# Kernel optimization log

Hardware: AMD Instinct MI355X
Metric: run time of the kernel (lower is better)

Reference implementation:

```python
import jax, jax.numpy as jnp
import numpy as np

B, NP, NM, C, H = 4, 256, 128, 128, 128
EPS = 1e-5

def layernorm(x, g, b):
    mu = jnp.mean(x, axis=-1, keepdims=True)
    var = jnp.var(x, axis=-1, keepdims=True)
    return (x - mu) * jax.lax.rsqrt(var + EPS) * g + b

def setup_inputs() -> dict:
    key = jax.random.key(0)
    ks = jax.random.split(key, 16)
    s = lambda d: 1.0 / np.sqrt(d)
    return {
        "z": jax.random.normal(ks[0], (B, NP, NM, C), jnp.float32),
        "z_mask": jnp.ones((B, NP, NM), jnp.float32),
        "pocket_pair": jax.random.normal(ks[1], (B, NP, NP, C), jnp.float32),
        "mol_pair": jax.random.normal(ks[2], (B, NM, NM, C), jnp.float32),
        "ln_g": jnp.ones((C,), jnp.float32), "ln_b": jnp.zeros((C,), jnp.float32),
        "lnh_g": jnp.ones((H,), jnp.float32), "lnh_b": jnp.zeros((H,), jnp.float32),
        "gw1": jax.random.uniform(ks[3], (C, H), jnp.float32, -s(C), s(C)),
        "gb1": jnp.zeros((H,), jnp.float32),
        "gw2": jax.random.uniform(ks[4], (C, H), jnp.float32, -s(C), s(C)),
        "gb2": jnp.zeros((H,), jnp.float32),
        "w1": jax.random.uniform(ks[5], (C, H), jnp.float32, -s(C), s(C)),
        "b1": jnp.zeros((H,), jnp.float32),
        "w2": jax.random.uniform(ks[6], (C, H), jnp.float32, -s(C), s(C)),
        "b2": jnp.zeros((H,), jnp.float32),
        "egw": jax.random.uniform(ks[7], (C, C), jnp.float32, -s(C), s(C)),
        "egb": jnp.zeros((C,), jnp.float32),
        "asw": jax.random.uniform(ks[8], (H, C), jnp.float32, -s(H), s(H)),
        "asb": jnp.zeros((C,), jnp.float32),
    }

def reference(z, z_mask, pocket_pair, mol_pair, ln_g, ln_b, lnh_g, lnh_b,
              gw1, gb1, gw2, gb2, w1, b1, w2, b2, egw, egb, asw, asb):
    m = z_mask[..., None]                      # [b,Np,Nm,1]
    zn = layernorm(z, ln_g, ln_b)              # [b,Np,Nm,C]
    pp = layernorm(pocket_pair, ln_g, ln_b)    # [b,Np,Np,C]
    mp = layernorm(mol_pair, ln_g, ln_b)       # [b,Nm,Nm,C]
    gate1 = lambda x: jax.nn.sigmoid(x @ gw1 + gb1) * (x @ w1 + b1)
    gate2 = lambda x: jax.nn.sigmoid(x @ gw2 + gb2) * (x @ w2 + b2)
    ab1 = gate1(zn) * m                        # [b,Np,Nm,H]
    ab2 = gate2(zn) * m                        # [b,Np,Nm,H]
    ppg = gate2(pp)                            # [b,Np,Np,H]
    mpg = gate1(mp)                            # [b,Nm,Nm,H]
    block1 = jnp.einsum('bikc,bkjc->bijc', ppg, ab1)   # [b,Np,Nm,H]
    block2 = jnp.einsum('bikc,bjkc->bijc', ab2, mpg)   # [b,Np,Nm,H]
    h = layernorm(block1 + block2, lnh_g, lnh_b)
    out = jax.nn.sigmoid(zn @ egw + egb) * (h @ asw + asb) * m
    return out
```

## Files before the change

### kernel.cpp

```cpp
#include <hip/hip_runtime.h>
#include <hip/hip_bf16.h>

#define DEVFN __device__ __forceinline__
using bf16 = __hip_bfloat16;
typedef __attribute__((ext_vector_type(8))) short short8;
typedef __attribute__((ext_vector_type(4))) float f32x4;
typedef __attribute__((ext_vector_type(4))) unsigned short us4;

constexpr int BB = 4, NP = 256, NM = 128, CC = 128, HH = 128;
constexpr float EPS = 1e-5f;

#define MFMA16(a,b,c) __builtin_amdgcn_mfma_f32_16x16x32_bf16((a),(b),(c),0,0,0)

DEVFN unsigned short bfbits(float v){ union{ bf16 b; unsigned short s; } u; u.b = __float2bfloat16(v); return u.s; }
DEVFN float bits2f(unsigned short s){ union{ unsigned int i; float f; } u; u.i = ((unsigned)s) << 16; return u.f; }
DEVFN float sigm(float x){ return 1.0f / (1.0f + __expf(-x)); }

__global__ __launch_bounds__(256)
void prep_weights_kernel(const float* __restrict__ gw1, const float* __restrict__ w1,
                         const float* __restrict__ gw2, const float* __restrict__ w2,
                         const float* __restrict__ egw, const float* __restrict__ asw,
                         bf16* __restrict__ wt)
{
  __shared__ float wl[128][129];
  const int bx = blockIdx.x;
  const float* W = (bx==0)?gw1 : (bx==1)?w1 : (bx==2)?gw2 : (bx==3)?w2 : (bx==4)?egw : asw;
  const int t = threadIdx.x;
  for (int i = 0; i < 16; ++i){
    int idx = t + 256*i;
    int k = idx >> 5, n0 = (idx & 31) * 4;
    float4 v = *reinterpret_cast<const float4*>(W + k*128 + n0);
    wl[k][n0] = v.x; wl[k][n0+1] = v.y; wl[k][n0+2] = v.z; wl[k][n0+3] = v.w;
  }
  __syncthreads();
  short* o = reinterpret_cast<short*>(wt) + bx * 16384;
  const int n = t >> 1, kh = t & 1;
  #pragma unroll
  for (int j = 0; j < 8; ++j){
    short8 p;
    #pragma unroll
    for (int u = 0; u < 8; ++u) p[u] = (short)bfbits(wl[kh*64 + j*8 + u][n]);
    *reinterpret_cast<short8*>(o + n*128 + kh*64 + j*8) = p;
  }
}

struct GateSmem {
  short xs[128*128];
  float lgb[2][128];
  float mu[128], rs[128], mk[128];
};

DEVFN void gate_pass(const char* xb, const float* mk, int t, int b, long rowb, long R,
                     const short* wtg, const short* wtl,
                     const float* __restrict__ bgp, const float* __restrict__ blp,
                     bf16* __restrict__ outp)
{
  const int l = t & 63, w = t >> 6, lr = l & 15, lg = l >> 4;
  const int n0 = w * 32;
  short8 bgf[2][4], blf[2][4];
  #pragma unroll
  for (int nt = 0; nt < 2; ++nt)
    #pragma unroll
    for (int ks = 0; ks < 4; ++ks){
      int n = n0 + nt*16 + lr, ko = ks*32 + lg*8;
      bgf[nt][ks] = *reinterpret_cast<const short8*>(wtg + n*128 + ko);
      blf[nt][ks] = *reinterpret_cast<const short8*>(wtl + n*128 + ko);
    }
  float bgv[2] = { bgp[n0 + lr], bgp[n0 + 16 + lr] };
  float blv[2] = { blp[n0 + lr], blp[n0 + 16 + lr] };
  unsigned short* ob = reinterpret_cast<unsigned short*>(outp);

  for (int mt = 0; mt < 8; ++mt){
    f32x4 zv = {0.f,0.f,0.f,0.f};
    f32x4 ag0 = zv, ag1 = zv, al0 = zv, al1 = zv;
    #pragma unroll
    for (int ks = 0; ks < 4; ++ks){
      int m = mt*16 + lr, ko = ks*32 + lg*8;
      short8 a = *reinterpret_cast<const short8*>(xb + ((m*256 + ko*2) ^ ((m & 7) << 4)));
      ag0 = MFMA16(a, bgf[0][ks], ag0);
      ag1 = MFMA16(a, bgf[1][ks], ag1);
      al0 = MFMA16(a, blf[0][ks], al0);
      al1 = MFMA16(a, blf[1][ks], al1);
    }
    #pragma unroll
    for (int nt = 0; nt < 2; ++nt){
      f32x4 ag = nt ? ag1 : ag0, al = nt ? al1 : al0;
      int h = n0 + nt*16 + lr;
      us4 pk;
      #pragma unroll
      for (int rg = 0; rg < 4; ++rg){
        int rowl = mt*16 + lg*4 + rg;
        float val = sigm(ag[rg] + bgv[nt]) * (al[rg] + blv[nt]) * mk[rowl];
        pk[rg] = bfbits(val);
      }
      *reinterpret_cast<us4*>(ob + (long)(b*128 + h)*R + rowb + mt*16 + lg*4) = pk;
    }
  }
}

DEVFN void eg_pass(const char* xb, int t, int b, long rowb, long R,
                   const short* wtg, const float* __restrict__ bgp, bf16* __restrict__ outp)
{
  const int l = t & 63, w = t >> 6, lr = l & 15, lg = l >> 4;
  const int n0 = w * 32;
  short8 bgf[2][4];
  #pragma unroll
  for (int nt = 0; nt < 2; ++nt)
    #pragma unroll
    for (int ks = 0; ks < 4; ++ks){
      int n = n0 + nt*16 + lr, ko = ks*32 + lg*8;
      bgf[nt][ks] = *reinterpret_cast<const short8*>(wtg + n*128 + ko);
    }
  float bgv[2] = { bgp[n0 + lr], bgp[n0 + 16 + lr] };
  unsigned short* ob = reinterpret_cast<unsigned short*>(outp);

  for (int mt = 0; mt < 8; ++mt){
    f32x4 zv = {0.f,0.f,0.f,0.f};
    f32x4 ag0 = zv, ag1 = zv;
    #pragma unroll
    for (int ks = 0; ks < 4; ++ks){
      int m = mt*16 + lr, ko = ks*32 + lg*8;
      short8 a = *reinterpret_cast<const short8*>(xb + ((m*256 + ko*2) ^ ((m & 7) << 4)));
      ag0 = MFMA16(a, bgf[0][ks], ag0);
      ag1 = MFMA16(a, bgf[1][ks], ag1);
    }
    #pragma unroll
    for (int nt = 0; nt < 2; ++nt){
      f32x4 ag = nt ? ag1 : ag0;
      int h = n0 + nt*16 + lr;
      us4 pk;
      #pragma unroll
      for (int rg = 0; rg < 4; ++rg) pk[rg] = bfbits(sigm(ag[rg] + bgv[nt]));
      *reinterpret_cast<us4*>(ob + (long)(b*128 + h)*R + rowb + mt*16 + lg*4) = pk;
    }
  }
}

template<int NPASS>
__global__ __launch_bounds__(256, 3)
void gate_mfma_kernel(const float* __restrict__ x, const float* __restrict__ mask,
                      const float* __restrict__ lng, const float* __restrict__ lnb,
                      const bf16* __restrict__ wt,
                      int m1g, int m1l, const float* __restrict__ bg1p, const float* __restrict__ bl1p, bf16* __restrict__ o1,
                      int m2g, int m2l, const float* __restrict__ bg2p, const float* __restrict__ bl2p, bf16* __restrict__ o2,
                      const float* __restrict__ bgep, bf16* __restrict__ oe,
                      long R)
{
  __shared__ GateSmem sm;
  const int t = threadIdx.x;
  const long row0 = (long)blockIdx.x * 128;
  const int b = (int)(row0 / R);
  const long rowb = row0 - (long)b * R;

  if (t < 128){
    sm.lgb[0][t] = lng[t];
    sm.lgb[1][t] = lnb[t];
    sm.mk[t] = mask ? mask[row0 + t] : 1.0f;
  }
  const int r = t >> 1, hf = t & 1;
  const float4* xrow = reinterpret_cast<const float4*>(x + (row0 + r)*128 + hf*64);
  float4 vb[16];
  float s = 0.f, ss = 0.f;
  #pragma unroll
  for (int i = 0; i < 16; ++i){
    float4 v = xrow[i]; vb[i] = v;
    s  += v.x + v.y + v.z + v.w;
    ss += v.x*v.x + v.y*v.y + v.z*v.z + v.w*v.w;
  }
  s  += __shfl_xor(s, 1);
  ss += __shfl_xor(ss, 1);
  if (!hf){
    float mu = s * (1.f/128.f);
    float var = ss * (1.f/128.f) - mu*mu;
    sm.mu[r] = mu;
    sm.rs[r] = rsqrtf(var + EPS);
  }
  __syncthreads();
  {
    const float mu = sm.mu[r], rg = sm.rs[r];
    char* xb = reinterpret_cast<char*>(sm.xs);
    #pragma unroll
    for (int j = 0; j < 8; ++j){
      float4 a = vb[2*j], c2 = vb[2*j+1];
      float vv[8] = {a.x, a.y, a.z, a.w, c2.x, c2.y, c2.z, c2.w};
      short8 p;
      #pragma unroll
      for (int u = 0; u < 8; ++u){
        int ch = hf*64 + j*8 + u;
        p[u] = (short)bfbits((vv[u] - mu) * rg * sm.lgb[0][ch] + sm.lgb[1][ch]);
      }
      *reinterpret_cast<short8*>(xb + ((r*256 + hf*128 + j*16) ^ ((r & 7) << 4))) = p;
    }
  }
  __syncthreads();

  const char* xb = reinterpret_cast<const char*>(sm.xs);
  const short* wts = reinterpret_cast<const short*>(wt);
  gate_pass(xb, sm.mk, t, b, rowb, R, wts + m1g*16384, wts + m1l*16384, bg1p, bl1p, o1);
  if (NPASS == 3){
    gate_pass(xb, sm.mk, t, b, rowb, R, wts + m2g*16384, wts + m2l*16384, bg2p, bl2p, o2);
    eg_pass(xb, t, b, rowb, R, wts + 4*16384, bgep, oe);
  }
}

__global__ __launch_bounds__(256, 2)
void einsum_mfma_kernel(const bf16* __restrict__ ppg, const bf16* __restrict__ ab1,
                        const bf16* __restrict__ ab2, const bf16* __restrict__ mpg,
                        float* __restrict__ bsum)
{
  __shared__ short b1t[128*256];
  const int t = threadIdx.x, l = t & 63, w = t >> 6, lr = l & 15, lg = l >> 4;
  const int bc = blockIdx.x;
  const short* A1 = reinterpret_cast<const short*>(ppg) + (long)bc * (NP*NP);
  const short* B1 = reinterpret_cast<const short*>(ab1) + (long)bc * (NP*NM);
  const short* A2 = reinterpret_cast<const short*>(ab2) + (long)bc * (NP*NM);
  const short* B2 = reinterpret_cast<const short*>(mpg) + (long)bc * (NM*NM);

  char* lb = reinterpret_cast<char*>(b1t);
  for (int it = 0; it < 16; ++it){
    int idx = t + 256*it;
    int k = idx >> 4, j0 = (idx & 15) * 8;
    short8 v = *reinterpret_cast<const short8*>(B1 + idx*8);
    #pragma unroll
    for (int u = 0; u < 8; ++u){
      int j = j0 + u;
      *reinterpret_cast<short*>(lb + ((j*512 + k*2) ^ ((j & 7) << 4))) = v[u];
    }
  }
  __syncthreads();

  f32x4 zv = {0.f,0.f,0.f,0.f};
  f32x4 acc[4][8];
  #pragma unroll
  for (int i = 0; i < 4; ++i)
    #pragma unroll
    for (int j = 0; j < 8; ++j) acc[i][j] = zv;

  const int m0 = w * 64;
  for (int ks = 0; ks < 8; ++ks){
    int ko = ks*32 + lg*8;
    short8 af[4];
    #pragma unroll
    for (int mt = 0; mt < 4; ++mt)
      af[mt] = *reinterpret_cast<const short8*>(A1 + (m0 + mt*16 + lr)*256 + ko);
    short8 bf[8];
    #pragma unroll
    for (int nt = 0; nt < 8; ++nt){
      int n = nt*16 + lr;
      bf[nt] = *reinterpret_cast<const short8*>(lb + ((n*512 + ko*2) ^ ((n & 7) << 4)));
    }
    #pragma unroll
    for (int mt = 0; mt < 4; ++mt)
      #pragma unroll
      for (int nt = 0; nt < 8; ++nt)
        acc[mt][nt] = MFMA16(af[mt], bf[nt], acc[mt][nt]);
  }
  for (int ks = 0; ks < 4; ++ks){
    int ko = ks*32 + lg*8;
    short8 af[4];
    #pragma unroll
    for (int mt = 0; mt < 4; ++mt)
      af[mt] = *reinterpret_cast<const short8*>(A2 + (m0 + mt*16 + lr)*128 + ko);
    short8 bf[8];
    #pragma unroll
    for (int nt = 0; nt < 8; ++nt)
      bf[nt] = *reinterpret_cast<const short8*>(B2 + (nt*16 + lr)*128 + ko);
    #pragma unroll
    for (int mt = 0; mt < 4; ++mt)
      #pragma unroll
      for (int nt = 0; nt < 8; ++nt)
        acc[mt][nt] = MFMA16(af[mt], bf[nt], acc[mt][nt]);
  }
  float* out = bsum + (long)bc * (NP*NM);
  #pragma unroll
  for (int mt = 0; mt < 4; ++mt)
    #pragma unroll
    for (int nt = 0; nt < 8; ++nt)
      #pragma unroll
      for (int rg = 0; rg < 4; ++rg)
        out[(m0 + mt*16 + lg*4 + rg)*128 + nt*16 + lr] = acc[mt][nt][rg];
}

__global__ __launch_bounds__(256, 2)
void final_mfma_kernel(const float* __restrict__ bsum, const bf16* __restrict__ eg,
                       const float* __restrict__ mask,
                       const float* __restrict__ lnhg, const float* __restrict__ lnhb,
                       const bf16* __restrict__ wt, const float* __restrict__ asb,
                       float* __restrict__ out)
{
  __shared__ struct {
    float xsT[128][68];
    short xs[64*128];
    float lgb[2][128];
    float ps[4][64], pss[4][64];
    float mu[64], rs[64], mk[64];
  } sm;
  const int t = threadIdx.x, l = t & 63, w = t >> 6, lr = l & 15, lg = l >> 4;
  const long row0 = (long)blockIdx.x * 64;
  const int b = (int)(row0 >> 15);
  const long rowb = row0 & 32767;

  if (t < 128){ sm.lgb[0][t] = lnhg[t]; sm.lgb[1][t] = lnhb[t]; }
  if (t < 64) sm.mk[t] = mask[row0 + t];

  for (int i = 0; i < 8; ++i){
    int idx = t + 256*i;
    int c = idx >> 4, j4 = idx & 15;
    float4 v = *reinterpret_cast<const float4*>(bsum + (long)(b*128 + c)*32768 + rowb + j4*4);
    *reinterpret_cast<float4*>(&sm.xsT[c][j4*4]) = v;
  }
  __syncthreads();
  {
    int ij = t & 63, q = t >> 6;
    float s = 0.f, ss = 0.f;
    #pragma unroll
    for (int k = 0; k < 32; ++k){
      float v = sm.xsT[q*32 + k][ij];
      s += v; ss += v*v;
    }
    sm.ps[q][ij] = s; sm.pss[q][ij] = ss;
  }
  __syncthreads();
  if (t < 64){
    float s  = sm.ps[0][t] + sm.ps[1][t] + sm.ps[2][t] + sm.ps[3][t];
    float ss = sm.pss[0][t] + sm.pss[1][t] + sm.pss[2][t] + sm.pss[3][t];
    float mu = s * (1.f/128.f);
    float var = ss * (1.f/128.f) - mu*mu;
    sm.mu[t] = mu; sm.rs[t] = rsqrtf(var + EPS);
  }
  __syncthreads();
  {
    int ij = t & 63, q = t >> 6;
    float mu = sm.mu[ij], rg = sm.rs[ij];
    char* xb = reinterpret_cast<char*>(sm.xs);
    #pragma unroll
    for (int u = 0; u < 4; ++u){
      short8 p;
      #pragma unroll
      for (int e = 0; e < 8; ++e){
        int c = q*32 + u*8 + e;
        p[e] = (short)bfbits((sm.xsT[c][ij] - mu) * rg * sm.lgb[0][c] + sm.lgb[1][c]);
      }
      *reinterpret_cast<short8*>(xb + ((ij*256 + q*64 + u*16) ^ ((ij & 7) << 4))) = p;
    }
  }
  __syncthreads();

  const short* aswt = reinterpret_cast<const short*>(wt) + 5*16384;
  short8 bfr[8][4];
  #pragma unroll
  for (int nt = 0; nt < 8; ++nt)
    #pragma unroll
    for (int ks = 0; ks < 4; ++ks)
      bfr[nt][ks] = *reinterpret_cast<const short8*>(aswt + (nt*16 + lr)*128 + ks*32 + lg*8);

  f32x4 zv = {0.f,0.f,0.f,0.f};
  f32x4 acc[8];
  #pragma unroll
  for (int i = 0; i < 8; ++i) acc[i] = zv;
  const char* xb = reinterpret_cast<const char*>(sm.xs);
  #pragma unroll
  for (int ks = 0; ks < 4; ++ks){
    int m = w*16 + lr, ko = ks*32 + lg*8;
    short8 a = *reinterpret_cast<const short8*>(xb + ((m*256 + ko*2) ^ ((m & 7) << 4)));
    #pragma unroll
    for (int nt = 0; nt < 8; ++nt)
      acc[nt] = MFMA16(a, bfr[nt][ks], acc[nt]);
  }
  const unsigned short* egb = reinterpret_cast<const unsigned short*>(eg);
  #pragma unroll
  for (int nt = 0; nt < 8; ++nt){
    int co = nt*16 + lr;
    float bias = asb[co];
    us4 egv = *reinterpret_cast<const us4*>(egb + (long)(b*128 + co)*32768 + rowb + w*16 + lg*4);
    #pragma unroll
    for (int rg = 0; rg < 4; ++rg){
      int rowl = w*16 + lg*4 + rg;
      float val = bits2f(egv[rg]) * (acc[nt][rg] + bias) * sm.mk[rowl];
      out[(row0 + rowl)*128 + co] = val;
    }
  }
}

extern "C" void kernel_launch(void* const* d_in, const int* in_sizes, int n_in,
                              void* d_out, int out_size, void* d_ws, size_t ws_size,
                              hipStream_t stream)
{
  const float* z     = (const float*)d_in[0];
  const float* zmask = (const float*)d_in[1];
  const float* pp    = (const float*)d_in[2];
  const float* mp    = (const float*)d_in[3];
  const float* ln_g  = (const float*)d_in[4];
  const float* ln_b  = (const float*)d_in[5];
  const float* lnh_g = (const float*)d_in[6];
  const float* lnh_b = (const float*)d_in[7];
  const float* gw1   = (const float*)d_in[8];
  const float* gb1   = (const float*)d_in[9];
  const float* gw2   = (const float*)d_in[10];
  const float* gb2   = (const float*)d_in[11];
  const float* w1    = (const float*)d_in[12];
  const float* b1    = (const float*)d_in[13];
  const float* w2    = (const float*)d_in[14];
  const float* b2    = (const float*)d_in[15];
  const float* egw   = (const float*)d_in[16];
  const float* egb   = (const float*)d_in[17];
  const float* asw   = (const float*)d_in[18];
  const float* asb   = (const float*)d_in[19];
  float* out = (float*)d_out;

  const size_t ZE = (size_t)BB*NP*NM*HH;
  const size_t PE = (size_t)BB*NP*NP*HH;
  const size_t ME = (size_t)BB*NM*NM*HH;
  char* ws = (char*)d_ws;
  size_t off = 0;
  bf16* wt   = (bf16*)(ws + off); off += 6 * 16384 * 2;
  bf16* ab1  = (bf16*)(ws + off); off += ZE * 2;
  bf16* ab2  = (bf16*)(ws + off); off += ZE * 2;
  bf16* egp  = (bf16*)(ws + off); off += ZE * 2;
  bf16* ppg  = (bf16*)(ws + off); off += PE * 2;
  bf16* mpg  = (bf16*)(ws + off); off += ME * 2;
  float* bsum = (float*)(ws + off); off += ZE * 4;
  if (ws_size < off) return;

  prep_weights_kernel<<<6, 256, 0, stream>>>(gw1, w1, gw2, w2, egw, asw, wt);

  gate_mfma_kernel<3><<<(BB*NP*NM)/128, 256, 0, stream>>>(
      z, zmask, ln_g, ln_b, wt,
      0, 1, gb1, b1, ab1,
      2, 3, gb2, b2, ab2,
      egb, egp, (long)(NP*NM));
  gate_mfma_kernel<1><<<(BB*NP*NP)/128, 256, 0, stream>>>(
      pp, nullptr, ln_g, ln_b, wt,
      2, 3, gb2, b2, ppg,
      0, 0, nullptr, nullptr, nullptr,
      nullptr, nullptr, (long)(NP*NP));
  gate_mfma_kernel<1><<<(BB*NM*NM)/128, 256, 0, stream>>>(
      mp, nullptr, ln_g, ln_b, wt,
      0, 1, gb1, b1, mpg,
      0, 0, nullptr, nullptr, nullptr,
      nullptr, nullptr, (long)(NM*NM));

  einsum_mfma_kernel<<<BB*CC, 256, 0, stream>>>(ppg, ab1, ab2, mpg, bsum);

  final_mfma_kernel<<<(BB*NP*NM)/64, 256, 0, stream>>>(
      bsum, egp, zmask, lnh_g, lnh_b, wt, asb, out);
}
```

Baseline: 279.6 us.

## Merge gate kernels into one launch, shrink row tiles, store einsum sum as bf16

```diff
diff --git a/kernel.cpp b/kernel.cpp
--- a/kernel.cpp
+++ b/kernel.cpp
@@ -45,15 +45,15 @@
 }
 
 struct GateSmem {
-  short xs[128*128];
+  short xs[64*128];
   float lgb[2][128];
-  float mu[128], rs[128], mk[128];
+  float mk[64];
 };
 
-DEVFN void gate_pass(const char* xb, const float* mk, int t, int b, long rowb, long R,
-                     const short* wtg, const short* wtl,
-                     const float* __restrict__ bgp, const float* __restrict__ blp,
-                     bf16* __restrict__ outp)
+DEVFN void gate_pass64(const char* xb, const float* mk, int t, long obase, long R,
+                       const short* wtg, const short* wtl,
+                       const float* __restrict__ bgp, const float* __restrict__ blp,
+                       bf16* outp)
 {
   const int l = t & 63, w = t >> 6, lr = l & 15, lg = l >> 4;
   const int n0 = w * 32;
@@ -70,59 +70,61 @@
   float blv[2] = { blp[n0 + lr], blp[n0 + 16 + lr] };
   unsigned short* ob = reinterpret_cast<unsigned short*>(outp);
 
-  for (int mt = 0; mt < 8; ++mt){
+  #pragma unroll
+  for (int mt = 0; mt < 4; ++mt){
     f32x4 zv = {0.f,0.f,0.f,0.f};
     f32x4 ag0 = zv, ag1 = zv, al0 = zv, al1 = zv;
+    #pragma unroll
+    for (int ks = 0; ks < 4; ++ks){
+      int m = mt*16 + lr, ko = ks*32 + lg*8;
+      short8 a = *reinterpret_cast<const short8*>(xb + ((m*256 + ko*2) ^ ((m & 7) << 4)));
+      ag0 = MFMA16(a, bgf[0][ks], ag0);
+      al0 = MFMA16(a, blf[0][ks], al0);
+      ag1 = MFMA16(a, bgf[1][ks], ag1);
+      al1 = MFMA16(a, blf[1][ks], al1);
+    }
+    #pragma unroll
+    for (int nt = 0; nt < 2; ++nt){
+      f32x4 ag = nt ? ag1 : ag0, al = nt ? al1 : al0;
+      int h = n0 + nt*16 + lr;
+      us4 pk;
+      #pragma unroll
+      for (int rg = 0; rg < 4; ++rg){
+        int rowl = mt*16 + lg*4 + rg;
+        float val = sigm(ag[rg] + bgv[nt]) * (al[rg] + blv[nt]) * mk[rowl];
+        pk[rg] = bfbits(val);
+      }
+      *reinterpret_cast<us4*>(ob + obase + (long)h*R + mt*16 + lg*4) = pk;
+    }
+  }
+}
+
+DEVFN void eg_pass64(const char* xb, int t, long obase, long R,
+                     const short* wtg, const float* __restrict__ bgp, bf16* outp)
+{
+  const int l = t & 63, w = t >> 6, lr = l & 15, lg = l >> 4;
+  const int n0 = w * 32;
+  short8 bgf[2][4];
+  #pragma unroll
+  for (int nt = 0; nt < 2; ++nt)
+    #pragma unroll
+    for (int ks = 0; ks < 4; ++ks){
+      int n = n0 + nt*16 + lr, ko = ks*32 + lg*8;
+      bgf[nt][ks] = *reinterpret_cast<const short8*>(wtg + n*128 + ko);
+    }
+  float bgv[2] = { bgp[n0 + lr], bgp[n0 + 16 + lr] };
+  unsigned short* ob = reinterpret_cast<unsigned short*>(outp);
+
+  #pragma unroll
+  for (int mt = 0; mt < 4; ++mt){
+    f32x4 zv = {0.f,0.f,0.f,0.f};
+    f32x4 ag0 = zv, ag1 = zv;
     #pragma unroll
     for (int ks = 0; ks < 4; ++ks){
       int m = mt*16 + lr, ko = ks*32 + lg*8;
       short8 a = *reinterpret_cast<const short8*>(xb + ((m*256 + ko*2) ^ ((m & 7) << 4)));
       ag0 = MFMA16(a, bgf[0][ks], ag0);
       ag1 = MFMA16(a, bgf[1][ks], ag1);
-      al0 = MFMA16(a, blf[0][ks], al0);
-      al1 = MFMA16(a, blf[1][ks], al1);
-    }
-    #pragma unroll
-    for (int nt = 0; nt < 2; ++nt){
-      f32x4 ag = nt ? ag1 : ag0, al = nt ? al1 : al0;
-      int h = n0 + nt*16 + lr;
-      us4 pk;
-      #pragma unroll
-      for (int rg = 0; rg < 4; ++rg){
-        int rowl = mt*16 + lg*4 + rg;
-        float val = sigm(ag[rg] + bgv[nt]) * (al[rg] + blv[nt]) * mk[rowl];
-        pk[rg] = bfbits(val);
-      }
-      *reinterpret_cast<us4*>(ob + (long)(b*128 + h)*R + rowb + mt*16 + lg*4) = pk;
-    }
-  }
-}
-
-DEVFN void eg_pass(const char* xb, int t, int b, long rowb, long R,
-                   const short* wtg, const float* __restrict__ bgp, bf16* __restrict__ outp)
-{
-  const int l = t & 63, w = t >> 6, lr = l & 15, lg = l >> 4;
-  const int n0 = w * 32;
-  short8 bgf[2][4];
-  #pragma unroll
-  for (int nt = 0; nt < 2; ++nt)
-    #pragma unroll
-    for (int ks = 0; ks < 4; ++ks){
-      int n = n0 + nt*16 + lr, ko = ks*32 + lg*8;
-      bgf[nt][ks] = *reinterpret_cast<const short8*>(wtg + n*128 + ko);
-    }
-  float bgv[2] = { bgp[n0 + lr], bgp[n0 + 16 + lr] };
-  unsigned short* ob = reinterpret_cast<unsigned short*>(outp);
-
-  for (int mt = 0; mt < 8; ++mt){
-    f32x4 zv = {0.f,0.f,0.f,0.f};
-    f32x4 ag0 = zv, ag1 = zv;
-    #pragma unroll
-    for (int ks = 0; ks < 4; ++ks){
-      int m = mt*16 + lr, ko = ks*32 + lg*8;
-      short8 a = *reinterpret_cast<const short8*>(xb + ((m*256 + ko*2) ^ ((m & 7) << 4)));
-      ag0 = MFMA16(a, bgf[0][ks], ag0);
-      ag1 = MFMA16(a, bgf[1][ks], ag1);
     }
     #pragma unroll
     for (int nt = 0; nt < 2; ++nt){
@@ -131,82 +133,97 @@
       us4 pk;
       #pragma unroll
       for (int rg = 0; rg < 4; ++rg) pk[rg] = bfbits(sigm(ag[rg] + bgv[nt]));
-      *reinterpret_cast<us4*>(ob + (long)(b*128 + h)*R + rowb + mt*16 + lg*4) = pk;
-    }
-  }
-}
-
-template<int NPASS>
+      *reinterpret_cast<us4*>(ob + obase + (long)h*R + mt*16 + lg*4) = pk;
+    }
+  }
+}
+
+constexpr int NZB = (BB*NP*NM)/64;
+constexpr int NPB = (BB*NP*NP)/64;
+constexpr int NMB = (BB*NM*NM)/64;
+
 __global__ __launch_bounds__(256, 3)
-void gate_mfma_kernel(const float* __restrict__ x, const float* __restrict__ mask,
-                      const float* __restrict__ lng, const float* __restrict__ lnb,
-                      const bf16* __restrict__ wt,
-                      int m1g, int m1l, const float* __restrict__ bg1p, const float* __restrict__ bl1p, bf16* __restrict__ o1,
-                      int m2g, int m2l, const float* __restrict__ bg2p, const float* __restrict__ bl2p, bf16* __restrict__ o2,
-                      const float* __restrict__ bgep, bf16* __restrict__ oe,
-                      long R)
+void gate_all_kernel(const float* __restrict__ z, const float* __restrict__ zmask,
+                     const float* __restrict__ pp, const float* __restrict__ mp,
+                     const float* __restrict__ lng, const float* __restrict__ lnb,
+                     const bf16* __restrict__ wt,
+                     const float* __restrict__ gb1, const float* __restrict__ b1,
+                     const float* __restrict__ gb2, const float* __restrict__ b2,
+                     const float* __restrict__ egbv,
+                     bf16* ab1, bf16* ab2, bf16* egp, bf16* ppg, bf16* mpg)
 {
   __shared__ GateSmem sm;
   const int t = threadIdx.x;
-  const long row0 = (long)blockIdx.x * 128;
+  const short* wts = reinterpret_cast<const short*>(wt);
+
+  int bx = blockIdx.x;
+  const float* x; const float* mask = nullptr;
+  long R; int npass = 1;
+  const short *w1g, *w1l; const float *bg1v, *bl1v; bf16* o1;
+  if (bx < NZB){
+    x = z; mask = zmask; R = (long)NP*NM; npass = 3;
+    w1g = wts + 0*16384; w1l = wts + 1*16384; bg1v = gb1; bl1v = b1; o1 = ab1;
+  } else if (bx < NZB + NPB){
+    bx -= NZB; x = pp; R = (long)NP*NP;
+    w1g = wts + 2*16384; w1l = wts + 3*16384; bg1v = gb2; bl1v = b2; o1 = ppg;
+  } else {
+    bx -= NZB + NPB; x = mp; R = (long)NM*NM;
+    w1g = wts + 0*16384; w1l = wts + 1*16384; bg1v = gb1; bl1v = b1; o1 = mpg;
+  }
+  const long row0 = (long)bx * 64;
   const int b = (int)(row0 / R);
   const long rowb = row0 - (long)b * R;
-
-  if (t < 128){
-    sm.lgb[0][t] = lng[t];
-    sm.lgb[1][t] = lnb[t];
-    sm.mk[t] = mask ? mask[row0 + t] : 1.0f;
-  }
-  const int r = t >> 1, hf = t & 1;
-  const float4* xrow = reinterpret_cast<const float4*>(x + (row0 + r)*128 + hf*64);
-  float4 vb[16];
+  const long obase = (long)b * 128 * R + rowb;
+
+  if (t < 128){ sm.lgb[0][t] = lng[t]; sm.lgb[1][t] = lnb[t]; }
+  if (t < 64) sm.mk[t] = mask ? mask[row0 + t] : 1.0f;
+
+  const int r = t >> 2, hf = t & 3;
+  const float4* xrow = reinterpret_cast<const float4*>(x + (row0 + r)*128 + hf*32);
+  float4 vb[8];
   float s = 0.f, ss = 0.f;
   #pragma unroll
-  for (int i = 0; i < 16; ++i){
+  for (int i = 0; i < 8; ++i){
     float4 v = xrow[i]; vb[i] = v;
     s  += v.x + v.y + v.z + v.w;
     ss += v.x*v.x + v.y*v.y + v.z*v.z + v.w*v.w;
   }
-  s  += __shfl_xor(s, 1);
-  ss += __shfl_xor(ss, 1);
-  if (!hf){
-    float mu = s * (1.f/128.f);
-    float var = ss * (1.f/128.f) - mu*mu;
-    sm.mu[r] = mu;
-    sm.rs[r] = rsqrtf(var + EPS);
-  }
+  s += __shfl_xor(s, 1);  ss += __shfl_xor(ss, 1);
+  s += __shfl_xor(s, 2);  ss += __shfl_xor(ss, 2);
+  const float mu = s * (1.f/128.f);
+  const float rsg = rsqrtf(ss * (1.f/128.f) - mu*mu + EPS);
   __syncthreads();
   {
-    const float mu = sm.mu[r], rg = sm.rs[r];
     char* xb = reinterpret_cast<char*>(sm.xs);
     #pragma unroll
-    for (int j = 0; j < 8; ++j){
+    for (int j = 0; j < 4; ++j){
       float4 a = vb[2*j], c2 = vb[2*j+1];
       float vv[8] = {a.x, a.y, a.z, a.w, c2.x, c2.y, c2.z, c2.w};
       short8 p;
       #pragma unroll
       for (int u = 0; u < 8; ++u){
-        int ch = hf*64 + j*8 + u;
-        p[u] = (short)bfbits((vv[u] - mu) * rg * sm.lgb[0][ch] + sm.lgb[1][ch]);
+        int ch = hf*32 + j*8 + u;
+        p[u] = (short)bfbits((vv[u] - mu) * rsg * sm.lgb[0][ch] + sm.lgb[1][ch]);
       }
-      *reinterpret_cast<short8*>(xb + ((r*256 + hf*128 + j*16) ^ ((r & 7) << 4))) = p;
+      *reinterpret_cast<short8*>(xb + ((r*256 + hf*64 + j*16) ^ ((r & 7) << 4))) = p;
     }
   }
   __syncthreads();
 
   const char* xb = reinterpret_cast<const char*>(sm.xs);
-  const short* wts = reinterpret_cast<const short*>(wt);
-  gate_pass(xb, sm.mk, t, b, rowb, R, wts + m1g*16384, wts + m1l*16384, bg1p, bl1p, o1);
-  if (NPASS == 3){
-    gate_pass(xb, sm.mk, t, b, rowb, R, wts + m2g*16384, wts + m2l*16384, bg2p, bl2p, o2);
-    eg_pass(xb, t, b, rowb, R, wts + 4*16384, bgep, oe);
-  }
-}
+  gate_pass64(xb, sm.mk, t, obase, R, w1g, w1l, bg1v, bl1v, o1);
+  if (npass == 3){
+    gate_pass64(xb, sm.mk, t, obase, R, wts + 2*16384, wts + 3*16384, gb2, b2, ab2);
+    eg_pass64(xb, t, obase, R, wts + 4*16384, egbv, egp);
+  }
+}
+
+DEVFN int b1swz(int j){ return (((j & 7) ^ ((j >> 3) & 7)) << 4); }
 
 __global__ __launch_bounds__(256, 2)
 void einsum_mfma_kernel(const bf16* __restrict__ ppg, const bf16* __restrict__ ab1,
                         const bf16* __restrict__ ab2, const bf16* __restrict__ mpg,
-                        float* __restrict__ bsum)
+                        bf16* __restrict__ bsum)
 {
   __shared__ short b1t[128*256];
   const int t = threadIdx.x, l = t & 63, w = t >> 6, lr = l & 15, lg = l >> 4;
@@ -224,7 +241,7 @@
     #pragma unroll
     for (int u = 0; u < 8; ++u){
       int j = j0 + u;
-      *reinterpret_cast<short*>(lb + ((j*512 + k*2) ^ ((j & 7) << 4))) = v[u];
+      *reinterpret_cast<short*>(lb + ((j*512 + k*2) ^ b1swz(j))) = v[u];
     }
   }
   __syncthreads();
@@ -247,7 +264,7 @@
     #pragma unroll
     for (int nt = 0; nt < 8; ++nt){
       int n = nt*16 + lr;
-      bf[nt] = *reinterpret_cast<const short8*>(lb + ((n*512 + ko*2) ^ ((n & 7) << 4)));
+      bf[nt] = *reinterpret_cast<const short8*>(lb + ((n*512 + ko*2) ^ b1swz(n)));
     }
     #pragma unroll
     for (int mt = 0; mt < 4; ++mt)
@@ -271,25 +288,25 @@
       for (int nt = 0; nt < 8; ++nt)
         acc[mt][nt] = MFMA16(af[mt], bf[nt], acc[mt][nt]);
   }
-  float* out = bsum + (long)bc * (NP*NM);
+  unsigned short* out = reinterpret_cast<unsigned short*>(bsum) + (long)bc * (NP*NM);
   #pragma unroll
   for (int mt = 0; mt < 4; ++mt)
     #pragma unroll
     for (int nt = 0; nt < 8; ++nt)
       #pragma unroll
       for (int rg = 0; rg < 4; ++rg)
-        out[(m0 + mt*16 + lg*4 + rg)*128 + nt*16 + lr] = acc[mt][nt][rg];
+        out[(m0 + mt*16 + lg*4 + rg)*128 + nt*16 + lr] = bfbits(acc[mt][nt][rg]);
 }
 
 __global__ __launch_bounds__(256, 2)
-void final_mfma_kernel(const float* __restrict__ bsum, const bf16* __restrict__ eg,
+void final_mfma_kernel(const bf16* __restrict__ bsum, const bf16* __restrict__ eg,
                        const float* __restrict__ mask,
                        const float* __restrict__ lnhg, const float* __restrict__ lnhb,
                        const bf16* __restrict__ wt, const float* __restrict__ asb,
                        float* __restrict__ out)
 {
   __shared__ struct {
-    float xsT[128][68];
+    short xsT[128][72];
     short xs[64*128];
     float lgb[2][128];
     float ps[4][64], pss[4][64];
@@ -303,11 +320,13 @@
   if (t < 128){ sm.lgb[0][t] = lnhg[t]; sm.lgb[1][t] = lnhb[t]; }
   if (t < 64) sm.mk[t] = mask[row0 + t];
 
-  for (int i = 0; i < 8; ++i){
+  const short* bs = reinterpret_cast<const short*>(bsum);
+  #pragma unroll
+  for (int i = 0; i < 4; ++i){
     int idx = t + 256*i;
-    int c = idx >> 4, j4 = idx & 15;
-    float4 v = *reinterpret_cast<const float4*>(bsum + (long)(b*128 + c)*32768 + rowb + j4*4);
-    *reinterpret_cast<float4*>(&sm.xsT[c][j4*4]) = v;
+    int c = idx >> 3, j8 = idx & 7;
+    short8 v = *reinterpret_cast<const short8*>(bs + (long)(b*128 + c)*32768 + rowb + j8*8);
+    *reinterpret_cast<short8*>(&sm.xsT[c][j8*8]) = v;
   }
   __syncthreads();
   {
@@ -315,7 +334,7 @@
     float s = 0.f, ss = 0.f;
     #pragma unroll
     for (int k = 0; k < 32; ++k){
-      float v = sm.xsT[q*32 + k][ij];
+      float v = bits2f((unsigned short)sm.xsT[q*32 + k][ij]);
       s += v; ss += v*v;
     }
     sm.ps[q][ij] = s; sm.pss[q][ij] = ss;
@@ -331,7 +350,7 @@
   __syncthreads();
   {
     int ij = t & 63, q = t >> 6;
-    float mu = sm.mu[ij], rg = sm.rs[ij];
+    float mu = sm.mu[ij], rg2 = sm.rs[ij];
     char* xb = reinterpret_cast<char*>(sm.xs);
     #pragma unroll
     for (int u = 0; u < 4; ++u){
@@ -339,7 +358,8 @@
       #pragma unroll
       for (int e = 0; e < 8; ++e){
         int c = q*32 + u*8 + e;
-        p[e] = (short)bfbits((sm.xsT[c][ij] - mu) * rg * sm.lgb[0][c] + sm.lgb[1][c]);
+        float v = bits2f((unsigned short)sm.xsT[c][ij]);
+        p[e] = (short)bfbits((v - mu) * rg2 * sm.lgb[0][c] + sm.lgb[1][c]);
       }
       *reinterpret_cast<short8*>(xb + ((ij*256 + q*64 + u*16) ^ ((ij & 7) << 4))) = p;
     }
@@ -347,13 +367,6 @@
   __syncthreads();
 
   const short* aswt = reinterpret_cast<const short*>(wt) + 5*16384;
-  short8 bfr[8][4];
-  #pragma unroll
-  for (int nt = 0; nt < 8; ++nt)
-    #pragma unroll
-    for (int ks = 0; ks < 4; ++ks)
-      bfr[nt][ks] = *reinterpret_cast<const short8*>(aswt + (nt*16 + lr)*128 + ks*32 + lg*8);
-
   f32x4 zv = {0.f,0.f,0.f,0.f};
   f32x4 acc[8];
   #pragma unroll
@@ -364,15 +377,17 @@
     int m = w*16 + lr, ko = ks*32 + lg*8;
     short8 a = *reinterpret_cast<const short8*>(xb + ((m*256 + ko*2) ^ ((m & 7) << 4)));
     #pragma unroll
-    for (int nt = 0; nt < 8; ++nt)
-      acc[nt] = MFMA16(a, bfr[nt][ks], acc[nt]);
-  }
-  const unsigned short* egb = reinterpret_cast<const unsigned short*>(eg);
+    for (int nt = 0; nt < 8; ++nt){
+      short8 bfr = *reinterpret_cast<const short8*>(aswt + (nt*16 + lr)*128 + ko);
+      acc[nt] = MFMA16(a, bfr, acc[nt]);
+    }
+  }
+  const unsigned short* egb2 = reinterpret_cast<const unsigned short*>(eg);
   #pragma unroll
   for (int nt = 0; nt < 8; ++nt){
     int co = nt*16 + lr;
     float bias = asb[co];
-    us4 egv = *reinterpret_cast<const us4*>(egb + (long)(b*128 + co)*32768 + rowb + w*16 + lg*4);
+    us4 egv = *reinterpret_cast<const us4*>(egb2 + (long)(b*128 + co)*32768 + rowb + w*16 + lg*4);
     #pragma unroll
     for (int rg = 0; rg < 4; ++rg){
       int rowl = w*16 + lg*4 + rg;
@@ -419,26 +434,15 @@
   bf16* egp  = (bf16*)(ws + off); off += ZE * 2;
   bf16* ppg  = (bf16*)(ws + off); off += PE * 2;
   bf16* mpg  = (bf16*)(ws + off); off += ME * 2;
-  float* bsum = (float*)(ws + off); off += ZE * 4;
+  bf16* bsum = (bf16*)(ws + off); off += ZE * 2;
   if (ws_size < off) return;
 
   prep_weights_kernel<<<6, 256, 0, stream>>>(gw1, w1, gw2, w2, egw, asw, wt);
 
-  gate_mfma_kernel<3><<<(BB*NP*NM)/128, 256, 0, stream>>>(
-      z, zmask, ln_g, ln_b, wt,
-      0, 1, gb1, b1, ab1,
-      2, 3, gb2, b2, ab2,
-      egb, egp, (long)(NP*NM));
-  gate_mfma_kernel<1><<<(BB*NP*NP)/128, 256, 0, stream>>>(
-      pp, nullptr, ln_g, ln_b, wt,
-      2, 3, gb2, b2, ppg,
-      0, 0, nullptr, nullptr, nullptr,
-      nullptr, nullptr, (long)(NP*NP));
-  gate_mfma_kernel<1><<<(BB*NM*NM)/128, 256, 0, stream>>>(
-      mp, nullptr, ln_g, ln_b, wt,
-      0, 1, gb1, b1, mpg,
-      0, 0, nullptr, nullptr, nullptr,
-      nullptr, nullptr, (long)(NM*NM));
+  gate_all_kernel<<<NZB + NPB + NMB, 256, 0, stream>>>(
+      z, zmask, pp, mp, ln_g, ln_b, wt,
+      gb1, b1, gb2, b2, egb,
+      ab1, ab2, egp, ppg, mpg);
 
   einsum_mfma_kernel<<<BB*CC, 256, 0, stream>>>(ppg, ab1, ab2, mpg, bsum);
 
```

Result: slower. 306.2 us (+9.5%).
